# Optimization experiments

Hardware: AMD Instinct MI355X
Metric: run time of the kernel (lower is better)

The kernel has to match this reference:

```python
import jax, jax.numpy as jnp
import numpy as np

EPS = 1e-6
N_HEADS = 8


def causal_dot_product(q, k, v):
    # q,k: [n,h,l,d]; v: [n,h,l,m]
    kv = jnp.einsum('nhld,nhlm->nhldm', k, v)          # [n,h,l,d,m] (large, matches original)
    kv = jnp.cumsum(kv, axis=2)
    return jnp.einsum('nhld,nhldm->nhlm', q, kv)


def flow_attention_causal(queries, keys, values, Wq, bq, Wk, bk, Wv, bv, Wo, bo):
    B, L, _ = queries.shape
    H = N_HEADS
    # projections + split heads -> [B,H,L,Dh]
    def proj(x, W, b):
        y = x @ W + b
        return y.reshape(B, L, H, -1).transpose(0, 2, 1, 3)
    q = jax.nn.sigmoid(proj(queries, Wq, bq))
    k = jax.nn.sigmoid(proj(keys, Wk, bk))
    v = proj(values, Wv, bv)

    normal = (jnp.arange(L, dtype=q.dtype) + 1.0)[None, None, :]  # [1,1,L]

    sink_incoming = 1.0 / jnp.einsum('nhld,nhld->nhl', q + EPS, jnp.cumsum(k, axis=2) + EPS)
    source_outgoing = 1.0 / jnp.einsum('nhld,nhld->nhl', k + EPS, jnp.cumsum(q, axis=2) + EPS)
    sink_incoming = sink_incoming * normal
    source_outgoing = source_outgoing * normal

    conserved_sink = jnp.einsum('nhld,nhld->nhl', q + EPS,
                                jnp.cumsum(k * source_outgoing[..., None], axis=2) + EPS) / normal
    conserved_source = jnp.einsum('nhld,nhld->nhl', k + EPS,
                                  jnp.cumsum(q * sink_incoming[..., None], axis=2) + EPS) / normal
    conserved_source = jnp.clip(conserved_source, -1.0, 1.0)

    sink_allocation = jax.nn.sigmoid(conserved_sink)
    conserved_source = jnp.exp(conserved_source)
    source_competition = conserved_source / jnp.cumsum(conserved_source, axis=-1) * normal

    x = causal_dot_product(q * (sink_incoming / normal)[..., None],
                           k,
                           v * source_competition[..., None]) * sink_allocation[..., None]
    x = x.transpose(0, 2, 1, 3).reshape(B, L, -1)
    return x @ Wo + bo  # dropout is identity at eval


def setup_inputs() -> dict:
    key = jax.random.key(0)
    ks = jax.random.split(key, 11)
    B, L, Din, Dm, Dout = 2, 1024, 512, 512, 512
    s = 0.02
    return {
        'queries': jax.random.normal(ks[0], (B, L, Din), jnp.float32),
        'keys': jax.random.normal(ks[1], (B, L, Din), jnp.float32),
        'values': jax.random.normal(ks[2], (B, L, Din), jnp.float32),
        'Wq': jax.random.normal(ks[3], (Din, Dm), jnp.float32) * s,
        'bq': jnp.zeros((Dm,), jnp.float32),
        'Wk': jax.random.normal(ks[4], (Din, Dm), jnp.float32) * s,
        'bk': jnp.zeros((Dm,), jnp.float32),
        'Wv': jax.random.normal(ks[5], (Din, Dm), jnp.float32) * s,
        'bv': jnp.zeros((Dm,), jnp.float32),
        'Wo': jax.random.normal(ks[6], (Dm, Dout), jnp.float32) * s,
        'bo': jnp.zeros((Dout,), jnp.float32),
    }


def reference(queries, keys, values, Wq, bq, Wk, bk, Wv, bv, Wo, bo):
    return flow_attention_causal(queries, keys, values, Wq, bq, Wk, bk, Wv, bv, Wo, bo)
```

## Files before the change

kernel.cpp:

```cpp
#include <hip/hip_runtime.h>
#include <math.h>

#define EPSF 1e-6f

constexpr int B_  = 2;
constexpr int L_  = 1024;
constexpr int D_  = 512;
constexpr int H_  = 8;
constexpr int DH_ = 64;
constexpr int BL_ = B_ * L_;
constexpr int BH_ = B_ * H_;
constexpr int CT_ = 64;
constexpr int NC_ = L_ / CT_;

typedef __attribute__((ext_vector_type(8))) short bf16x8;
typedef __attribute__((ext_vector_type(4))) float f32x4;

__device__ __forceinline__ unsigned short f2bf(float f) {
  union { float f; unsigned int u; } v; v.f = f;
  const unsigned int u = v.u;
  return (unsigned short)((u + 0x7FFFu + ((u >> 16) & 1u)) >> 16);
}
__device__ __forceinline__ float bf2f(unsigned short u) {
  union { unsigned int u; float f; } v; v.u = ((unsigned int)u) << 16;
  return v.f;
}

__device__ __forceinline__ int sw(int row, int col) {
  return row * 64 + (col ^ ((row & 7) << 3));
}

__global__ __launch_bounds__(256) void proj3_k(const float* __restrict__ Qin,
                                               const float* __restrict__ Kin,
                                               const float* __restrict__ Vin,
                                               const float* __restrict__ Wq,
                                               const float* __restrict__ bq,
                                               const float* __restrict__ Wk,
                                               const float* __restrict__ bk,
                                               const float* __restrict__ Wv,
                                               const float* __restrict__ bv,
                                               unsigned short* __restrict__ Qb,
                                               unsigned short* __restrict__ Kb,
                                               unsigned short* __restrict__ Vb,
                                               float* __restrict__ sumQ,
                                               float* __restrict__ sumK) {
  const int z = blockIdx.z;
  const float* A    = (z == 0) ? Qin : (z == 1) ? Kin : Vin;
  const float* W    = (z == 0) ? Wq  : (z == 1) ? Wk  : Wv;
  const float* bias = (z == 0) ? bq  : (z == 1) ? bk  : bv;
  unsigned short* out = (z == 0) ? Qb : (z == 1) ? Kb : Vb;
  float* csum       = (z == 0) ? sumQ : (z == 1) ? sumK : nullptr;
  const bool sig = (z < 2);

  __shared__ __align__(16) short Als[64 * 72];
  __shared__ __align__(16) short Bls[64 * 72];
  const int tid = threadIdx.x;
  const int m0 = blockIdx.x * 64, n0 = blockIdx.y * 64;
  const int arow = tid >> 2, ak0 = (tid & 3) << 4;
  const int bcol = tid & 63, bk0 = (tid >> 6) << 4;
  const int lane = tid & 63, wid = tid >> 6;
  const int wr = wid >> 1, wc = wid & 1;
  const int lrow = lane & 15, lk = (lane >> 4) << 3;

  f32x4 acc[2][2] = {{{0.f, 0.f, 0.f, 0.f}, {0.f, 0.f, 0.f, 0.f}},
                     {{0.f, 0.f, 0.f, 0.f}, {0.f, 0.f, 0.f, 0.f}}};
  float ra[16], rb[16];

  auto loadAB = [&](int kt) {
#pragma unroll
    for (int j = 0; j < 4; ++j) {
      const float4 f = *(const float4*)&A[(size_t)(m0 + arow) * D_ + kt + ak0 + 4 * j];
      ra[4 * j + 0] = f.x; ra[4 * j + 1] = f.y; ra[4 * j + 2] = f.z; ra[4 * j + 3] = f.w;
    }
    const float* gw = &W[(size_t)(kt + bk0) * D_ + n0 + bcol];
#pragma unroll
    for (int j = 0; j < 16; ++j) rb[j] = gw[(size_t)j * D_];
  };
  auto writeLDS = [&]() {
    bf16x8 pa0, pa1, pb0, pb1;
#pragma unroll
    for (int j = 0; j < 8; ++j) {
      pa0[j] = (short)f2bf(ra[j]);
      pa1[j] = (short)f2bf(ra[j + 8]);
      pb0[j] = (short)f2bf(rb[j]);
      pb1[j] = (short)f2bf(rb[j + 8]);
    }
    *(bf16x8*)&Als[arow * 72 + ak0] = pa0;
    *(bf16x8*)&Als[arow * 72 + ak0 + 8] = pa1;
    *(bf16x8*)&Bls[bcol * 72 + bk0] = pb0;
    *(bf16x8*)&Bls[bcol * 72 + bk0 + 8] = pb1;
  };
  auto compute = [&]() {
#pragma unroll
    for (int ks = 0; ks < 2; ++ks) {
      const int ko = ks * 32 + lk;
      bf16x8 a0 = *(const bf16x8*)&Als[(wr * 32 + lrow) * 72 + ko];
      bf16x8 a1 = *(const bf16x8*)&Als[(wr * 32 + 16 + lrow) * 72 + ko];
      bf16x8 b0 = *(const bf16x8*)&Bls[(wc * 32 + lrow) * 72 + ko];
      bf16x8 b1 = *(const bf16x8*)&Bls[(wc * 32 + 16 + lrow) * 72 + ko];
      acc[0][0] = __builtin_amdgcn_mfma_f32_16x16x32_bf16(a0, b0, acc[0][0], 0, 0, 0);
      acc[0][1] = __builtin_amdgcn_mfma_f32_16x16x32_bf16(a0, b1, acc[0][1], 0, 0, 0);
      acc[1][0] = __builtin_amdgcn_mfma_f32_16x16x32_bf16(a1, b0, acc[1][0], 0, 0, 0);
      acc[1][1] = __builtin_amdgcn_mfma_f32_16x16x32_bf16(a1, b1, acc[1][1], 0, 0, 0);
    }
  };

  loadAB(0);
  writeLDS();
  for (int kt = 64; kt < D_; kt += 64) {
    loadAB(kt);
    __syncthreads();
    compute();
    __syncthreads();
    writeLDS();
  }
  __syncthreads();
  compute();

  const int b = m0 >> 10, h = n0 >> 6;
  float psum[2] = {0.f, 0.f};
#pragma unroll
  for (int j = 0; j < 2; ++j) {
    const int col = n0 + wc * 32 + j * 16 + lrow;
    const float bv4 = bias[col];
    const int dh = col & 63;
#pragma unroll
    for (int i = 0; i < 2; ++i) {
#pragma unroll
      for (int r = 0; r < 4; ++r) {
        const int row = m0 + wr * 32 + i * 16 + (lane >> 4) * 4 + r;
        float x = acc[i][j][r] + bv4;
        if (sig) x = 1.0f / (1.0f + expf(-x));
        const unsigned short ub = f2bf(x);
        const int l = row & (L_ - 1);
        out[(((size_t)(b * H_ + h)) * L_ + l) * DH_ + dh] = ub;
        psum[j] += bf2f(ub);
      }
    }
  }
  if (csum) {
    float* sumS = (float*)Als;
#pragma unroll
    for (int j = 0; j < 2; ++j) {
      psum[j] += __shfl_xor(psum[j], 16);
      psum[j] += __shfl_xor(psum[j], 32);
      if ((lane >> 4) == 0) sumS[wr * 64 + wc * 32 + j * 16 + lrow] = psum[j];
    }
    __syncthreads();
    if (tid < 64) {
      const int c = (m0 & (L_ - 1)) >> 6;
      const int bc = (b * H_ + h) * NC_ + c;
      csum[bc * DH_ + tid] = sumS[tid] + sumS[64 + tid];
    }
  }
}

__global__ __launch_bounds__(1024) void flow_phase1_k(const unsigned short* __restrict__ Qb,
                                                      const unsigned short* __restrict__ Kb,
                                                      const float* __restrict__ sumQ,
                                                      const float* __restrict__ sumK,
                                                      float* __restrict__ qscale,
                                                      float* __restrict__ si_a,
                                                      float* __restrict__ so_a,
                                                      float* __restrict__ sumQSI,
                                                      float* __restrict__ sumKSO) {
  const int bc = blockIdx.x, bh = bc >> 4, c = bc & (NC_ - 1);
  const int g = bc * CT_;
  const int tid = threadIdx.x, lane = tid & 63, w = tid >> 6;
  __shared__ float qS[64][65], kS[64][65];
  __shared__ float pqS[64], pkS[64];
  __shared__ float aS[16][64], bS[16][64];
  __shared__ float siS[64], soS[64];
  if (tid < 512) {
    const int row = tid >> 3, d0 = (tid & 7) << 3;
    const bf16x8 qv = *(const bf16x8*)&Qb[(size_t)g * DH_ + tid * 8];
    const bf16x8 kv = *(const bf16x8*)&Kb[(size_t)g * DH_ + tid * 8];
#pragma unroll
    for (int j = 0; j < 8; ++j) {
      qS[row][d0 + j] = bf2f((unsigned short)qv[j]);
      kS[row][d0 + j] = bf2f((unsigned short)kv[j]);
    }
  } else if (tid < 576) {
    const int d = tid - 512;
    float pq = 0.f, pk = 0.f;
    for (int cc = 0; cc < c; ++cc) {
      pq += sumQ[(bh * NC_ + cc) * DH_ + d];
      pk += sumK[(bh * NC_ + cc) * DH_ + d];
    }
    pqS[d] = pq; pkS[d] = pk;
  }
  __syncthreads();
  float ap = 0.f, bp = 0.f;
#pragma unroll
  for (int dd = 0; dd < 4; ++dd) {
    const int d = w * 4 + dd;
    const float qv = qS[lane][d];
    const float kv = kS[lane][d];
    float ck = kv, cq = qv;
#pragma unroll
    for (int off = 1; off < 64; off <<= 1) {
      const float t1 = __shfl_up(ck, off);
      const float t2 = __shfl_up(cq, off);
      ck += (lane >= off) ? t1 : 0.f;
      cq += (lane >= off) ? t2 : 0.f;
    }
    ck += pkS[d];
    cq += pqS[d];
    ap += (qv + EPSF) * (ck + EPSF);
    bp += (kv + EPSF) * (cq + EPSF);
  }
  aS[w][lane] = ap; bS[w][lane] = bp;
  __syncthreads();
  if (tid < 64) {
    float a = 0.f, b = 0.f;
#pragma unroll
    for (int ww = 0; ww < 16; ++ww) { a += aS[ww][tid]; b += bS[ww][tid]; }
    const float normal = (float)(c * CT_ + tid + 1);
    const float si = normal / a, so = normal / b;
    qscale[g + tid] = 1.0f / a;
    si_a[g + tid] = si;
    so_a[g + tid] = so;
    siS[tid] = si; soS[tid] = so;
  }
  __syncthreads();
  float sq = 0.f, sk = 0.f;
#pragma unroll
  for (int li = 0; li < 4; ++li) {
    const int l = w * 4 + li;
    sq += qS[l][lane] * siS[l];
    sk += kS[l][lane] * soS[l];
  }
  aS[w][lane] = sq; bS[w][lane] = sk;
  __syncthreads();
  if (tid < 64) {
    float s1 = 0.f, s2 = 0.f;
#pragma unroll
    for (int ww = 0; ww < 16; ++ww) { s1 += aS[ww][tid]; s2 += bS[ww][tid]; }
    sumQSI[bc * DH_ + tid] = s1;
    sumKSO[bc * DH_ + tid] = s2;
  }
}

__global__ __launch_bounds__(1024) void flow_phase2_k(const unsigned short* __restrict__ Qb,
                                                      const unsigned short* __restrict__ Kb,
                                                      const float* __restrict__ sumQSI,
                                                      const float* __restrict__ sumKSO,
                                                      const float* __restrict__ si_a,
                                                      const float* __restrict__ so_a,
                                                      float* __restrict__ salloc,
                                                      float* __restrict__ e_a,
                                                      float* __restrict__ sumE) {
  const int bc = blockIdx.x, bh = bc >> 4, c = bc & (NC_ - 1);
  const int g = bc * CT_;
  const int tid = threadIdx.x, lane = tid & 63, w = tid >> 6;
  __shared__ float qS[64][65], kS[64][65];
  __shared__ float pqS[64], pkS[64];
  __shared__ float aS[16][64], bS[16][64];
  if (tid < 512) {
    const int row = tid >> 3, d0 = (tid & 7) << 3;
    const bf16x8 qv = *(const bf16x8*)&Qb[(size_t)g * DH_ + tid * 8];
    const bf16x8 kv = *(const bf16x8*)&Kb[(size_t)g * DH_ + tid * 8];
#pragma unroll
    for (int j = 0; j < 8; ++j) {
      qS[row][d0 + j] = bf2f((unsigned short)qv[j]);
      kS[row][d0 + j] = bf2f((unsigned short)kv[j]);
    }
  } else if (tid < 576) {
    const int d = tid - 512;
    float pq = 0.f, pk = 0.f;
    for (int cc = 0; cc < c; ++cc) {
      pq += sumQSI[(bh * NC_ + cc) * DH_ + d];
      pk += sumKSO[(bh * NC_ + cc) * DH_ + d];
    }
    pqS[d] = pq; pkS[d] = pk;
  }
  __syncthreads();
  const float si = si_a[g + lane];
  const float so = so_a[g + lane];
  float c1p = 0.f, c2p = 0.f;
#pragma unroll
  for (int dd = 0; dd < 4; ++dd) {
    const int d = w * 4 + dd;
    const float qv = qS[lane][d];
    const float kv = kS[lane][d];
    float ckso = kv * so, cqsi = qv * si;
#pragma unroll
    for (int off = 1; off < 64; off <<= 1) {
      const float t1 = __shfl_up(ckso, off);
      const float t2 = __shfl_up(cqsi, off);
      ckso += (lane >= off) ? t1 : 0.f;
      cqsi += (lane >= off) ? t2 : 0.f;
    }
    ckso += pkS[d];
    cqsi += pqS[d];
    c1p += (qv + EPSF) * (ckso + EPSF);
    c2p += (kv + EPSF) * (cqsi + EPSF);
  }
  aS[w][lane] = c1p; bS[w][lane] = c2p;
  __syncthreads();
  if (tid < 64) {
    float c1 = 0.f, c2 = 0.f;
#pragma unroll
    for (int ww = 0; ww < 16; ++ww) { c1 += aS[ww][tid]; c2 += bS[ww][tid]; }
    const float normal = (float)(c * CT_ + tid + 1);
    const float cs_sink = c1 / normal;
    salloc[g + tid] = 1.0f / (1.0f + expf(-cs_sink));
    float cs_src = c2 / normal;
    cs_src = fminf(1.0f, fmaxf(-1.0f, cs_src));
    const float e = expf(cs_src);
    e_a[g + tid] = e;
    float tot = e;
#pragma unroll
    for (int off = 32; off; off >>= 1) tot += __shfl_xor(tot, off);
    if (tid == 0) sumE[bc] = tot;
  }
}

__global__ __launch_bounds__(256) void flow_ckv_k(const unsigned short* __restrict__ K16,
                                                  const unsigned short* __restrict__ V16,
                                                  const float* __restrict__ e_a,
                                                  const float* __restrict__ sumE,
                                                  float* __restrict__ comp,
                                                  float* __restrict__ KV) {
  const int bc = blockIdx.x, bh = bc >> 4, c = bc & (NC_ - 1);
  const int g = bc * CT_;
  const int tid = threadIdx.x;
  __shared__ float compS[CT_];
  __shared__ __align__(16) unsigned short kT16[64 * 64];
  __shared__ __align__(16) unsigned short vT16[64 * 64];
  if (tid < 64) {
    const int lane = tid;
    const float e = e_a[g + lane];
    float se = (lane < c) ? sumE[bh * NC_ + lane] : 0.f;
#pragma unroll
    for (int off = 32; off; off >>= 1) se += __shfl_xor(se, off);
    float s = e;
#pragma unroll
    for (int off = 1; off < 64; off <<= 1) {
      const float t = __shfl_up(s, off);
      s += (lane >= off) ? t : 0.f;
    }
    const float cf = e / (se + s) * (float)(c * CT_ + lane + 1);
    compS[lane] = cf;
    comp[g + lane] = cf;
  }
  __syncthreads();
#pragma unroll
  for (int it = 0; it < 2; ++it) {
    const int i8 = it * 256 + tid;
    const int l = i8 >> 3, d0 = (i8 & 7) << 3;
    const bf16x8 kv = *(const bf16x8*)&K16[(size_t)g * DH_ + i8 * 8];
    const bf16x8 vv = *(const bf16x8*)&V16[(size_t)g * DH_ + i8 * 8];
    const float cl = compS[l];
#pragma unroll
    for (int j = 0; j < 8; ++j) {
      kT16[sw(d0 + j, l)] = (unsigned short)kv[j];
      vT16[sw(d0 + j, l)] = f2bf(bf2f((unsigned short)vv[j]) * cl);
    }
  }
  __syncthreads();
  const int lane = tid & 63, w = tid >> 6;
  const int fr = lane & 15, fk = (lane >> 4) << 3;
  f32x4 acc[4] = {{0.f, 0.f, 0.f, 0.f}, {0.f, 0.f, 0.f, 0.f},
                  {0.f, 0.f, 0.f, 0.f}, {0.f, 0.f, 0.f, 0.f}};
  const bf16x8 a0 = *(const bf16x8*)&kT16[sw(w * 16 + fr, fk)];
  const bf16x8 a1 = *(const bf16x8*)&kT16[sw(w * 16 + fr, fk + 32)];
#pragma unroll
  for (int cb = 0; cb < 4; ++cb) {
    const bf16x8 b0 = *(const bf16x8*)&vT16[sw(cb * 16 + fr, fk)];
    const bf16x8 b1 = *(const bf16x8*)&vT16[sw(cb * 16 + fr, fk + 32)];
    acc[cb] = __builtin_amdgcn_mfma_f32_16x16x32_bf16(a0, b0, acc[cb], 0, 0, 0);
    acc[cb] = __builtin_amdgcn_mfma_f32_16x16x32_bf16(a1, b1, acc[cb], 0, 0, 0);
  }
  float* outp = KV + (size_t)bc * DH_ * DH_;
#pragma unroll
  for (int r = 0; r < 4; ++r) {
    const int d = w * 16 + (lane >> 4) * 4 + r;
#pragma unroll
    for (int cb = 0; cb < 4; ++cb) outp[d * DH_ + cb * 16 + fr] = acc[cb][r];
  }
}

__global__ __launch_bounds__(256) void attn_k(const unsigned short* __restrict__ Q16,
                                              const unsigned short* __restrict__ K16,
                                              const unsigned short* __restrict__ V16,
                                              const float* __restrict__ KVraw,
                                              const float* __restrict__ qscale,
                                              const float* __restrict__ salloc,
                                              const float* __restrict__ comp,
                                              unsigned short* __restrict__ X) {
  const int bc = blockIdx.x;
  const int bh = bc >> 4, c = bc & (NC_ - 1);
  const int bb = bh >> 3, hh = bh & (H_ - 1);
  const int g = bc * CT_;
  __shared__ __align__(16) unsigned short qp16[64 * 64];
  __shared__ __align__(16) unsigned short k16[64 * 64];
  __shared__ __align__(16) unsigned short vT16[64 * 64];
  __shared__ __align__(16) unsigned short kvT16[64 * 64];
  __shared__ __align__(16) unsigned short S16[64 * 64];
  const int tid = threadIdx.x;
#pragma unroll
  for (int it = 0; it < 2; ++it) {
    const int i8 = it * 256 + tid;
    const int r = i8 >> 3, d0 = (i8 & 7) << 3;
    const bf16x8 qv = *(const bf16x8*)&Q16[(size_t)g * DH_ + i8 * 8];
    const bf16x8 kv = *(const bf16x8*)&K16[(size_t)g * DH_ + i8 * 8];
    const bf16x8 vv = *(const bf16x8*)&V16[(size_t)g * DH_ + i8 * 8];
    const float qs = qscale[g + r];
    const float cl = comp[g + r];
    bf16x8 pq;
#pragma unroll
    for (int j = 0; j < 8; ++j) pq[j] = (short)f2bf(bf2f((unsigned short)qv[j]) * qs);
    *(bf16x8*)&qp16[sw(r, d0)] = pq;
    *(bf16x8*)&k16[sw(r, d0)] = kv;
#pragma unroll
    for (int j = 0; j < 8; ++j)
      vT16[sw(d0 + j, r)] = f2bf(bf2f((unsigned short)vv[j]) * cl);
  }
  {
    const float* kvbh = KVraw + (size_t)bh * NC_ * DH_ * DH_;
    for (int i4 = tid; i4 < DH_ * DH_ / 4; i4 += 256) {
      const int d = i4 >> 4, mg = (i4 & 15) << 2;
      float s0 = 0.f, s1 = 0.f, s2 = 0.f, s3 = 0.f;
#pragma unroll
      for (int cc = 0; cc < NC_; ++cc) {
        const float4 t = *(const float4*)&kvbh[(size_t)cc * (DH_ * DH_) + d * DH_ + mg];
        const float msk = (cc < c) ? 1.f : 0.f;
        s0 += t.x * msk; s1 += t.y * msk; s2 += t.z * msk; s3 += t.w * msk;
      }
      kvT16[sw(mg + 0, d)] = f2bf(s0);
      kvT16[sw(mg + 1, d)] = f2bf(s1);
      kvT16[sw(mg + 2, d)] = f2bf(s2);
      kvT16[sw(mg + 3, d)] = f2bf(s3);
    }
  }
  __syncthreads();

  const int lane = tid & 63, w = tid >> 6;
  const int fr = lane & 15, fk = (lane >> 4) << 3;
  const int arow = w * 16 + fr;
  f32x4 accX[4] = {{0.f, 0.f, 0.f, 0.f}, {0.f, 0.f, 0.f, 0.f},
                   {0.f, 0.f, 0.f, 0.f}, {0.f, 0.f, 0.f, 0.f}};
  f32x4 accS[4] = {{0.f, 0.f, 0.f, 0.f}, {0.f, 0.f, 0.f, 0.f},
                   {0.f, 0.f, 0.f, 0.f}, {0.f, 0.f, 0.f, 0.f}};

  const bf16x8 aq0 = *(const bf16x8*)&qp16[sw(arow, fk)];
  const bf16x8 aq1 = *(const bf16x8*)&qp16[sw(arow, fk + 32)];
#pragma unroll
  for (int cb = 0; cb < 4; ++cb) {
    const int bcol = cb * 16 + fr;
    const bf16x8 bv0 = *(const bf16x8*)&kvT16[sw(bcol, fk)];
    const bf16x8 bv1 = *(const bf16x8*)&kvT16[sw(bcol, fk + 32)];
    accX[cb] = __builtin_amdgcn_mfma_f32_16x16x32_bf16(aq0, bv0, accX[cb], 0, 0, 0);
    accX[cb] = __builtin_amdgcn_mfma_f32_16x16x32_bf16(aq1, bv1, accX[cb], 0, 0, 0);
    const bf16x8 bk0 = *(const bf16x8*)&k16[sw(bcol, fk)];
    const bf16x8 bk1 = *(const bf16x8*)&k16[sw(bcol, fk + 32)];
    accS[cb] = __builtin_amdgcn_mfma_f32_16x16x32_bf16(aq0, bk0, accS[cb], 0, 0, 0);
    accS[cb] = __builtin_amdgcn_mfma_f32_16x16x32_bf16(aq1, bk1, accS[cb], 0, 0, 0);
  }
#pragma unroll
  for (int cb = 0; cb < 4; ++cb) {
#pragma unroll
    for (int r = 0; r < 4; ++r) {
      const int l = w * 16 + (lane >> 4) * 4 + r;
      const int j = cb * 16 + fr;
      S16[sw(l, j)] = (j <= l) ? f2bf(accS[cb][r]) : (unsigned short)0;
    }
  }
  __syncthreads();
  const bf16x8 as0 = *(const bf16x8*)&S16[sw(arow, fk)];
  const bf16x8 as1 = *(const bf16x8*)&S16[sw(arow, fk + 32)];
#pragma unroll
  for (int cb = 0; cb < 4; ++cb) {
    const int bcol = cb * 16 + fr;
    const bf16x8 bv0 = *(const bf16x8*)&vT16[sw(bcol, fk)];
    const bf16x8 bv1 = *(const bf16x8*)&vT16[sw(bcol, fk + 32)];
    accX[cb] = __builtin_amdgcn_mfma_f32_16x16x32_bf16(as0, bv0, accX[cb], 0, 0, 0);
    accX[cb] = __builtin_amdgcn_mfma_f32_16x16x32_bf16(as1, bv1, accX[cb], 0, 0, 0);
  }
#pragma unroll
  for (int r = 0; r < 4; ++r) {
    const int l = w * 16 + (lane >> 4) * 4 + r;
    const float sal = salloc[g + l];
    const size_t rowbase = ((size_t)(bb * L_ + c * CT_ + l)) * D_ + hh * DH_;
#pragma unroll
    for (int cb = 0; cb < 4; ++cb) {
      const int m = cb * 16 + fr;
      X[rowbase + m] = f2bf(accX[cb][r] * sal);
    }
  }
}

__global__ __launch_bounds__(256) void gemm_out_k(const unsigned short* __restrict__ A,
                                                  const float* __restrict__ W,
                                                  const float* __restrict__ bias,
                                                  float* __restrict__ out) {
  __shared__ __align__(16) short Als[64 * 72];
  __shared__ __align__(16) short Bls[64 * 72];
  const int tid = threadIdx.x;
  const int m0 = blockIdx.x * 64, n0 = blockIdx.y * 64;
  const int arow = tid >> 2, ak0 = (tid & 3) << 4;
  const int bcol = tid & 63, bk0 = (tid >> 6) << 4;
  const int lane = tid & 63, wid = tid >> 6;
  const int wr = wid >> 1, wc = wid & 1;
  const int lrow = lane & 15, lk = (lane >> 4) << 3;

  f32x4 acc[2][2] = {{{0.f, 0.f, 0.f, 0.f}, {0.f, 0.f, 0.f, 0.f}},
                     {{0.f, 0.f, 0.f, 0.f}, {0.f, 0.f, 0.f, 0.f}}};
  bf16x8 pa0, pa1;
  float rb[16];
  auto loadAB = [&](int kt) {
    pa0 = *(const bf16x8*)&A[(size_t)(m0 + arow) * D_ + kt + ak0];
    pa1 = *(const bf16x8*)&A[(size_t)(m0 + arow) * D_ + kt + ak0 + 8];
    const float* gw = &W[(size_t)(kt + bk0) * D_ + n0 + bcol];
#pragma unroll
    for (int j = 0; j < 16; ++j) rb[j] = gw[(size_t)j * D_];
  };
  auto writeLDS = [&]() {
    bf16x8 pb0, pb1;
#pragma unroll
    for (int j = 0; j < 8; ++j) {
      pb0[j] = (short)f2bf(rb[j]);
      pb1[j] = (short)f2bf(rb[j + 8]);
    }
    *(bf16x8*)&Als[arow * 72 + ak0] = pa0;
    *(bf16x8*)&Als[arow * 72 + ak0 + 8] = pa1;
    *(bf16x8*)&Bls[bcol * 72 + bk0] = pb0;
    *(bf16x8*)&Bls[bcol * 72 + bk0 + 8] = pb1;
  };
  auto compute = [&]() {
#pragma unroll
    for (int ks = 0; ks < 2; ++ks) {
      const int ko = ks * 32 + lk;
      bf16x8 a0 = *(const bf16x8*)&Als[(wr * 32 + lrow) * 72 + ko];
      bf16x8 a1 = *(const bf16x8*)&Als[(wr * 32 + 16 + lrow) * 72 + ko];
      bf16x8 b0 = *(const bf16x8*)&Bls[(wc * 32 + lrow) * 72 + ko];
      bf16x8 b1 = *(const bf16x8*)&Bls[(wc * 32 + 16 + lrow) * 72 + ko];
      acc[0][0] = __builtin_amdgcn_mfma_f32_16x16x32_bf16(a0, b0, acc[0][0], 0, 0, 0);
      acc[0][1] = __builtin_amdgcn_mfma_f32_16x16x32_bf16(a0, b1, acc[0][1], 0, 0, 0);
      acc[1][0] = __builtin_amdgcn_mfma_f32_16x16x32_bf16(a1, b0, acc[1][0], 0, 0, 0);
      acc[1][1] = __builtin_amdgcn_mfma_f32_16x16x32_bf16(a1, b1, acc[1][1], 0, 0, 0);
    }
  };

  loadAB(0);
  writeLDS();
  for (int kt = 64; kt < D_; kt += 64) {
    loadAB(kt);
    __syncthreads();
    compute();
    __syncthreads();
    writeLDS();
  }
  __syncthreads();
  compute();

#pragma unroll
  for (int j = 0; j < 2; ++j) {
    const int col = n0 + wc * 32 + j * 16 + lrow;
    const float bv4 = bias[col];
#pragma unroll
    for (int i = 0; i < 2; ++i) {
#pragma unroll
      for (int r = 0; r < 4; ++r) {
        const int row = m0 + wr * 32 + i * 16 + (lane >> 4) * 4 + r;
        out[(size_t)row * D_ + col] = acc[i][j][r] + bv4;
      }
    }
  }
}

extern "C" void kernel_launch(void* const* d_in, const int* in_sizes, int n_in,
                              void* d_out, int out_size, void* d_ws, size_t ws_size,
                              hipStream_t stream) {
  (void)in_sizes; (void)n_in; (void)out_size; (void)ws_size;
  const float* queries = (const float*)d_in[0];
  const float* keys    = (const float*)d_in[1];
  const float* values  = (const float*)d_in[2];
  const float* Wq = (const float*)d_in[3];
  const float* bq = (const float*)d_in[4];
  const float* Wk = (const float*)d_in[5];
  const float* bk = (const float*)d_in[6];
  const float* Wv = (const float*)d_in[7];
  const float* bv = (const float*)d_in[8];
  const float* Wo = (const float*)d_in[9];
  const float* bo = (const float*)d_in[10];

  const size_t seg = (size_t)BH_ * L_ * DH_;
  unsigned short* Qb = (unsigned short*)d_ws;
  unsigned short* Kb = Qb + seg;
  unsigned short* Vb = Kb + seg;
  float* KVb = (float*)(Vb + seg);
  float* p   = KVb + (size_t)BH_ * NC_ * DH_ * DH_;
  float* qscale = p; p += BH_ * L_;
  float* salloc = p; p += BH_ * L_;
  float* comp   = p; p += BH_ * L_;
  float* si_a   = p; p += BH_ * L_;
  float* so_a   = p; p += BH_ * L_;
  float* e_a    = p; p += BH_ * L_;
  float* sumQ   = p; p += BH_ * NC_ * DH_;
  float* sumK   = p; p += BH_ * NC_ * DH_;
  float* sumQSI = p; p += BH_ * NC_ * DH_;
  float* sumKSO = p; p += BH_ * NC_ * DH_;
  float* sumE   = p; p += BH_ * NC_;
  unsigned short* Xb16 = (unsigned short*)p;

  proj3_k<<<dim3(BL_ / 64, D_ / 64, 3), 256, 0, stream>>>(
      queries, keys, values, Wq, bq, Wk, bk, Wv, bv, Qb, Kb, Vb, sumQ, sumK);
  flow_phase1_k<<<BH_ * NC_, 1024, 0, stream>>>(Qb, Kb, sumQ, sumK,
                                                qscale, si_a, so_a, sumQSI, sumKSO);
  flow_phase2_k<<<BH_ * NC_, 1024, 0, stream>>>(Qb, Kb, sumQSI, sumKSO, si_a, so_a,
                                                salloc, e_a, sumE);
  flow_ckv_k<<<BH_ * NC_, 256, 0, stream>>>(Kb, Vb, e_a, sumE, comp, KVb);
  attn_k<<<BH_ * NC_, 256, 0, stream>>>(Qb, Kb, Vb, KVb, qscale, salloc, comp, Xb16);
  gemm_out_k<<<dim3(BL_ / 64, D_ / 64), 256, 0, stream>>>(Xb16, Wo, bo, (float*)d_out);
}
```

Before: 57.81 us.

## Double threads per block in ckv and attention kernels, splitting MFMA work across waves

Measured after the change: 56.42 us. 2.4% less time.

```diff
diff --git a/kernel.cpp b/kernel.cpp
--- a/kernel.cpp
+++ b/kernel.cpp
@@ -316,7 +316,7 @@
   }
 }
 
-__global__ __launch_bounds__(256) void flow_ckv_k(const unsigned short* __restrict__ K16,
+__global__ __launch_bounds__(512) void flow_ckv_k(const unsigned short* __restrict__ K16,
                                                   const unsigned short* __restrict__ V16,
                                                   const float* __restrict__ e_a,
                                                   const float* __restrict__ sumE,
@@ -345,9 +345,8 @@
     comp[g + lane] = cf;
   }
   __syncthreads();
-#pragma unroll
-  for (int it = 0; it < 2; ++it) {
-    const int i8 = it * 256 + tid;
+  {
+    const int i8 = tid;
     const int l = i8 >> 3, d0 = (i8 & 7) << 3;
     const bf16x8 kv = *(const bf16x8*)&K16[(size_t)g * DH_ + i8 * 8];
     const bf16x8 vv = *(const bf16x8*)&V16[(size_t)g * DH_ + i8 * 8];
@@ -360,28 +359,30 @@
   }
   __syncthreads();
   const int lane = tid & 63, w = tid >> 6;
+  const int wr2 = w >> 1, wc2 = w & 1;
   const int fr = lane & 15, fk = (lane >> 4) << 3;
-  f32x4 acc[4] = {{0.f, 0.f, 0.f, 0.f}, {0.f, 0.f, 0.f, 0.f},
-                  {0.f, 0.f, 0.f, 0.f}, {0.f, 0.f, 0.f, 0.f}};
-  const bf16x8 a0 = *(const bf16x8*)&kT16[sw(w * 16 + fr, fk)];
-  const bf16x8 a1 = *(const bf16x8*)&kT16[sw(w * 16 + fr, fk + 32)];
-#pragma unroll
-  for (int cb = 0; cb < 4; ++cb) {
-    const bf16x8 b0 = *(const bf16x8*)&vT16[sw(cb * 16 + fr, fk)];
-    const bf16x8 b1 = *(const bf16x8*)&vT16[sw(cb * 16 + fr, fk + 32)];
+  f32x4 acc[2] = {{0.f, 0.f, 0.f, 0.f}, {0.f, 0.f, 0.f, 0.f}};
+  const bf16x8 a0 = *(const bf16x8*)&kT16[sw(wr2 * 16 + fr, fk)];
+  const bf16x8 a1 = *(const bf16x8*)&kT16[sw(wr2 * 16 + fr, fk + 32)];
+#pragma unroll
+  for (int cb = 0; cb < 2; ++cb) {
+    const int bcol = wc2 * 32 + cb * 16 + fr;
+    const bf16x8 b0 = *(const bf16x8*)&vT16[sw(bcol, fk)];
+    const bf16x8 b1 = *(const bf16x8*)&vT16[sw(bcol, fk + 32)];
     acc[cb] = __builtin_amdgcn_mfma_f32_16x16x32_bf16(a0, b0, acc[cb], 0, 0, 0);
     acc[cb] = __builtin_amdgcn_mfma_f32_16x16x32_bf16(a1, b1, acc[cb], 0, 0, 0);
   }
   float* outp = KV + (size_t)bc * DH_ * DH_;
 #pragma unroll
   for (int r = 0; r < 4; ++r) {
-    const int d = w * 16 + (lane >> 4) * 4 + r;
-#pragma unroll
-    for (int cb = 0; cb < 4; ++cb) outp[d * DH_ + cb * 16 + fr] = acc[cb][r];
-  }
-}
-
-__global__ __launch_bounds__(256) void attn_k(const unsigned short* __restrict__ Q16,
+    const int d = wr2 * 16 + (lane >> 4) * 4 + r;
+#pragma unroll
+    for (int cb = 0; cb < 2; ++cb)
+      outp[d * DH_ + wc2 * 32 + cb * 16 + fr] = acc[cb][r];
+  }
+}
+
+__global__ __launch_bounds__(512) void attn_k(const unsigned short* __restrict__ Q16,
                                               const unsigned short* __restrict__ K16,
                                               const unsigned short* __restrict__ V16,
                                               const float* __restrict__ KVraw,
@@ -399,9 +400,8 @@
   __shared__ __align__(16) unsigned short kvT16[64 * 64];
   __shared__ __align__(16) unsigned short S16[64 * 64];
   const int tid = threadIdx.x;
-#pragma unroll
-  for (int it = 0; it < 2; ++it) {
-    const int i8 = it * 256 + tid;
+  {
+    const int i8 = tid;
     const int r = i8 >> 3, d0 = (i8 & 7) << 3;
     const bf16x8 qv = *(const bf16x8*)&Q16[(size_t)g * DH_ + i8 * 8];
     const bf16x8 kv = *(const bf16x8*)&K16[(size_t)g * DH_ + i8 * 8];
@@ -419,7 +419,9 @@
   }
   {
     const float* kvbh = KVraw + (size_t)bh * NC_ * DH_ * DH_;
-    for (int i4 = tid; i4 < DH_ * DH_ / 4; i4 += 256) {
+#pragma unroll
+    for (int it = 0; it < 2; ++it) {
+      const int i4 = it * 512 + tid;
       const int d = i4 >> 4, mg = (i4 & 15) << 2;
       float s0 = 0.f, s1 = 0.f, s2 = 0.f, s3 = 0.f;
 #pragma unroll
@@ -438,55 +440,65 @@
 
   const int lane = tid & 63, w = tid >> 6;
   const int fr = lane & 15, fk = (lane >> 4) << 3;
-  const int arow = w * 16 + fr;
+  const int wS = (w >= 4) ? (w - 4) : w;
+  const int arow = wS * 16 + fr;
+  const bf16x8 aq0 = *(const bf16x8*)&qp16[sw(arow, fk)];
+  const bf16x8 aq1 = *(const bf16x8*)&qp16[sw(arow, fk + 32)];
+
   f32x4 accX[4] = {{0.f, 0.f, 0.f, 0.f}, {0.f, 0.f, 0.f, 0.f},
                    {0.f, 0.f, 0.f, 0.f}, {0.f, 0.f, 0.f, 0.f}};
-  f32x4 accS[4] = {{0.f, 0.f, 0.f, 0.f}, {0.f, 0.f, 0.f, 0.f},
-                   {0.f, 0.f, 0.f, 0.f}, {0.f, 0.f, 0.f, 0.f}};
-
-  const bf16x8 aq0 = *(const bf16x8*)&qp16[sw(arow, fk)];
-  const bf16x8 aq1 = *(const bf16x8*)&qp16[sw(arow, fk + 32)];
-#pragma unroll
-  for (int cb = 0; cb < 4; ++cb) {
-    const int bcol = cb * 16 + fr;
-    const bf16x8 bv0 = *(const bf16x8*)&kvT16[sw(bcol, fk)];
-    const bf16x8 bv1 = *(const bf16x8*)&kvT16[sw(bcol, fk + 32)];
-    accX[cb] = __builtin_amdgcn_mfma_f32_16x16x32_bf16(aq0, bv0, accX[cb], 0, 0, 0);
-    accX[cb] = __builtin_amdgcn_mfma_f32_16x16x32_bf16(aq1, bv1, accX[cb], 0, 0, 0);
-    const bf16x8 bk0 = *(const bf16x8*)&k16[sw(bcol, fk)];
-    const bf16x8 bk1 = *(const bf16x8*)&k16[sw(bcol, fk + 32)];
-    accS[cb] = __builtin_amdgcn_mfma_f32_16x16x32_bf16(aq0, bk0, accS[cb], 0, 0, 0);
-    accS[cb] = __builtin_amdgcn_mfma_f32_16x16x32_bf16(aq1, bk1, accS[cb], 0, 0, 0);
-  }
-#pragma unroll
-  for (int cb = 0; cb < 4; ++cb) {
+  if (w < 4) {
+#pragma unroll
+    for (int cb = 0; cb < 4; ++cb) {
+      const int bcol = cb * 16 + fr;
+      const bf16x8 bv0 = *(const bf16x8*)&kvT16[sw(bcol, fk)];
+      const bf16x8 bv1 = *(const bf16x8*)&kvT16[sw(bcol, fk + 32)];
+      accX[cb] = __builtin_amdgcn_mfma_f32_16x16x32_bf16(aq0, bv0, accX[cb], 0, 0, 0);
+      accX[cb] = __builtin_amdgcn_mfma_f32_16x16x32_bf16(aq1, bv1, accX[cb], 0, 0, 0);
+    }
+  } else {
+    f32x4 accS[4] = {{0.f, 0.f, 0.f, 0.f}, {0.f, 0.f, 0.f, 0.f},
+                     {0.f, 0.f, 0.f, 0.f}, {0.f, 0.f, 0.f, 0.f}};
+#pragma unroll
+    for (int cb = 0; cb < 4; ++cb) {
+      const int bcol = cb * 16 + fr;
+      const bf16x8 bk0 = *(const bf16x8*)&k16[sw(bcol, fk)];
+      const bf16x8 bk1 = *(const bf16x8*)&k16[sw(bcol, fk + 32)];
+      accS[cb] = __builtin_amdgcn_mfma_f32_16x16x32_bf16(aq0, bk0, accS[cb], 0, 0, 0);
+      accS[cb] = __builtin_amdgcn_mfma_f32_16x16x32_bf16(aq1, bk1, accS[cb], 0, 0, 0);
+    }
+#pragma unroll
+    for (int cb = 0; cb < 4; ++cb) {
+#pragma unroll
+      for (int r = 0; r < 4; ++r) {
+        const int l = wS * 16 + (lane >> 4) * 4 + r;
+        const int j = cb * 16 + fr;
+        S16[sw(l, j)] = (j <= l) ? f2bf(accS[cb][r]) : (unsigned short)0;
+      }
+    }
+  }
+  __syncthreads();
+  if (w < 4) {
+    const bf16x8 as0 = *(const bf16x8*)&S16[sw(arow, fk)];
+    const bf16x8 as1 = *(const bf16x8*)&S16[sw(arow, fk + 32)];
+#pragma unroll
+    for (int cb = 0; cb < 4; ++cb) {
+      const int bcol = cb * 16 + fr;
+      const bf16x8 bv0 = *(const bf16x8*)&vT16[sw(bcol, fk)];
+      const bf16x8 bv1 = *(const bf16x8*)&vT16[sw(bcol, fk + 32)];
+      accX[cb] = __builtin_amdgcn_mfma_f32_16x16x32_bf16(as0, bv0, accX[cb], 0, 0, 0);
+      accX[cb] = __builtin_amdgcn_mfma_f32_16x16x32_bf16(as1, bv1, accX[cb], 0, 0, 0);
+    }
 #pragma unroll
     for (int r = 0; r < 4; ++r) {
-      const int l = w * 16 + (lane >> 4) * 4 + r;
-      const int j = cb * 16 + fr;
-      S16[sw(l, j)] = (j <= l) ? f2bf(accS[cb][r]) : (unsigned short)0;
-    }
-  }
-  __syncthreads();
-  const bf16x8 as0 = *(const bf16x8*)&S16[sw(arow, fk)];
-  const bf16x8 as1 = *(const bf16x8*)&S16[sw(arow, fk + 32)];
-#pragma unroll
-  for (int cb = 0; cb < 4; ++cb) {
-    const int bcol = cb * 16 + fr;
-    const bf16x8 bv0 = *(const bf16x8*)&vT16[sw(bcol, fk)];
-    const bf16x8 bv1 = *(const bf16x8*)&vT16[sw(bcol, fk + 32)];
-    accX[cb] = __builtin_amdgcn_mfma_f32_16x16x32_bf16(as0, bv0, accX[cb], 0, 0, 0);
-    accX[cb] = __builtin_amdgcn_mfma_f32_16x16x32_bf16(as1, bv1, accX[cb], 0, 0, 0);
-  }
-#pragma unroll
-  for (int r = 0; r < 4; ++r) {
-    const int l = w * 16 + (lane >> 4) * 4 + r;
-    const float sal = salloc[g + l];
-    const size_t rowbase = ((size_t)(bb * L_ + c * CT_ + l)) * D_ + hh * DH_;
-#pragma unroll
-    for (int cb = 0; cb < 4; ++cb) {
-      const int m = cb * 16 + fr;
-      X[rowbase + m] = f2bf(accX[cb][r] * sal);
+      const int l = wS * 16 + (lane >> 4) * 4 + r;
+      const float sal = salloc[g + l];
+      const size_t rowbase = ((size_t)(bb * L_ + c * CT_ + l)) * D_ + hh * DH_;
+#pragma unroll
+      for (int cb = 0; cb < 4; ++cb) {
+        const int m = cb * 16 + fr;
+        X[rowbase + m] = f2bf(accX[cb][r] * sal);
+      }
     }
   }
 }
@@ -611,7 +623,7 @@
                                                 qscale, si_a, so_a, sumQSI, sumKSO);
   flow_phase2_k<<<BH_ * NC_, 1024, 0, stream>>>(Qb, Kb, sumQSI, sumKSO, si_a, so_a,
                                                 salloc, e_a, sumE);
-  flow_ckv_k<<<BH_ * NC_, 256, 0, stream>>>(Kb, Vb, e_a, sumE, comp, KVb);
-  attn_k<<<BH_ * NC_, 256, 0, stream>>>(Qb, Kb, Vb, KVb, qscale, salloc, comp, Xb16);
+  flow_ckv_k<<<BH_ * NC_, 512, 0, stream>>>(Kb, Vb, e_a, sumE, comp, KVb);
+  attn_k<<<BH_ * NC_, 512, 0, stream>>>(Qb, Kb, Vb, KVb, qscale, salloc, comp, Xb16);
   gemm_out_k<<<dim3(BL_ / 64, D_ / 64), 256, 0, stream>>>(Xb16, Wo, bo, (float*)d_out);
 }
```
